# Kernel tuning notes

Measured on AMD Instinct MI355X. Metric: run time of the kernel, lower is better.

Reference implementation:

```python
import jax, jax.numpy as jnp
import numpy as np

B, N = 16, 16384
K = 16        # num_keypoints
LATENT = 128
CAGE = 8
BN_EPS = 1e-5


def setup_inputs():
    key = jax.random.key(0)
    ks = jax.random.split(key, 40)
    def rn(i, shape, s=1.0):
        return jax.random.normal(ks[i], shape, dtype=jnp.float32) * s
    inp = {
        "source_points": rn(0, (B, N, 3)),
        "target_points": rn(1, (B, N, 3)),
        "enc_w1": rn(2, (64, 3), 0.3), "enc_b1": rn(3, (64,), 0.1),
        "bn1_gamma": 1.0 + rn(4, (64,), 0.1), "bn1_beta": rn(5, (64,), 0.1),
        "bn1_mean": rn(6, (64,), 0.1), "bn1_var": 0.5 + jax.random.uniform(ks[7], (64,), dtype=jnp.float32),
        "enc_w2": rn(8, (128, 64), 0.1), "enc_b2": rn(9, (128,), 0.1),
        "bn2_gamma": 1.0 + rn(10, (128,), 0.1), "bn2_beta": rn(11, (128,), 0.1),
        "bn2_mean": rn(12, (128,), 0.1), "bn2_var": 0.5 + jax.random.uniform(ks[13], (128,), dtype=jnp.float32),
        "enc_w3": rn(14, (LATENT, 128), 0.1), "enc_b3": rn(15, (LATENT,), 0.1),
        "bn3_gamma": 1.0 + rn(16, (LATENT,), 0.1), "bn3_beta": rn(17, (LATENT,), 0.1),
        "bn3_mean": rn(18, (LATENT,), 0.1), "bn3_var": 0.5 + jax.random.uniform(ks[19], (LATENT,), dtype=jnp.float32),
        "kp_w1": rn(20, (128, LATENT), 0.1), "kp_b1": rn(21, (128,), 0.1),
        "kp_w2": rn(22, (K * 3, 128), 0.1), "kp_b2": rn(23, (K * 3,), 0.1),
        "cg_w1": rn(24, (128, K * 3), 0.1), "cg_b1": rn(25, (128,), 0.1),
        "cg_w2": rn(26, (CAGE ** 3 * 3, 128), 0.05), "cg_b2": rn(27, (CAGE ** 3 * 3,), 0.01),
    }
    return inp


def _bn(x, g, b, m, v):
    # inference-mode BatchNorm1d over channel (last) dim
    return (x - m) * jax.lax.rsqrt(v + BN_EPS) * g + b


def _encode(pts, w1, b1, g1, be1, m1, v1, w2, b2, g2, be2, m2, v2, w3, b3, g3, be3, m3, v3):
    # pointwise 1x1 convs == per-point linear layers; pts: (B, N, 3)
    h = jax.nn.relu(_bn(jnp.einsum('bnc,oc->bno', pts, w1) + b1, g1, be1, m1, v1))
    h = jax.nn.relu(_bn(jnp.einsum('bnc,oc->bno', h, w2) + b2, g2, be2, m2, v2))
    h = jax.nn.relu(_bn(jnp.einsum('bnc,oc->bno', h, w3) + b3, g3, be3, m3, v3))
    return h.max(axis=1)  # global max-pool -> (B, LATENT)


def _fps_one(pts, kps):
    # pts: (N,3), kps: (K,3). Same math as the torch loop: iterative farthest-point
    # selection; recomputing cdist to selected[:i] each step == incremental min-dist.
    # squared distances preserve argmax/min of euclidean distances.
    d0 = jnp.sum((pts[:, None, :] - kps[None, :, :]) ** 2, -1).min(axis=1)
    sel0 = pts[jnp.argmax(d0)]
    mind = jnp.sum((pts - sel0) ** 2, -1)
    def step(mind, _):
        sel = pts[jnp.argmax(mind)]
        return jnp.minimum(mind, jnp.sum((pts - sel) ** 2, -1)), sel
    _, sels = jax.lax.scan(step, mind, None, length=K - 1)
    return jnp.concatenate([sel0[None], sels], axis=0)  # (K, 3)


def _fps(points, keypoints):
    return jax.vmap(_fps_one)(points, keypoints)


def _cage_deform(pts, disp):
    # pts: (B,N,3), disp: (B,C,C,C,3). Batched trilinear interpolation on the cage.
    C = CAGE
    lin = jnp.linspace(0.0, 1.0, C)
    grid = jnp.stack(jnp.meshgrid(lin, lin, lin, indexing='ij'), axis=-1)
    cage = grid[None] + disp
    cf = cage.reshape(cage.shape[0], C * C * C, 3)
    pmin = pts.min(axis=1, keepdims=True)
    pmax = pts.max(axis=1, keepdims=True)
    t = (pts - pmin) / (pmax - pmin + 1e-6) * (C - 1)
    idx = jnp.clip(t.astype(jnp.int32), 0, C - 2)   # trunc == floor (t >= 0)
    w = t - idx.astype(t.dtype)
    u, v, z = idx[..., 0], idx[..., 1], idx[..., 2]
    wx, wy, wz = w[..., 0:1], w[..., 1:2], w[..., 2:3]
    def corner(du, dv, dz):
        flat = (u + du) * C * C + (v + dv) * C + (z + dz)      # (B,N)
        flat = jnp.broadcast_to(flat[..., None], flat.shape + (3,))
        return jnp.take_along_axis(cf, flat, axis=1)            # (B,N,3)
    d = ((1 - wx) * (1 - wy) * (1 - wz) * corner(0, 0, 0)
         + wx * (1 - wy) * (1 - wz) * corner(1, 0, 0)
         + (1 - wx) * wy * (1 - wz) * corner(0, 1, 0)
         + wx * wy * (1 - wz) * corner(1, 1, 0)
         + (1 - wx) * (1 - wy) * wz * corner(0, 0, 1)
         + wx * (1 - wy) * wz * corner(1, 0, 1)
         + (1 - wx) * wy * wz * corner(0, 1, 1)
         + wx * wy * wz * corner(1, 1, 1))
    return pts + d


def reference(source_points, target_points, enc_w1, enc_b1, bn1_gamma, bn1_beta, bn1_mean, bn1_var, enc_w2, enc_b2, bn2_gamma, bn2_beta, bn2_mean, bn2_var, enc_w3, enc_b3, bn3_gamma, bn3_beta, bn3_mean, bn3_var, kp_w1, kp_b1, kp_w2, kp_b2, cg_w1, cg_b1, cg_w2, cg_b2):
    enc = lambda p: _encode(p, enc_w1, enc_b1, bn1_gamma, bn1_beta, bn1_mean, bn1_var,
                            enc_w2, enc_b2, bn2_gamma, bn2_beta, bn2_mean, bn2_var,
                            enc_w3, enc_b3, bn3_gamma, bn3_beta, bn3_mean, bn3_var)
    src_lat = enc(source_points)
    tgt_lat = enc(target_points)
    kp = lambda lat: (jax.nn.relu(lat @ kp_w1.T + kp_b1) @ kp_w2.T + kp_b2).reshape(-1, K, 3)
    src_kp = _fps(source_points, kp(src_lat))
    tgt_kp = _fps(target_points, kp(tgt_lat))
    diff = (tgt_kp - src_kp).reshape(-1, K * 3)
    disp = (jax.nn.relu(diff @ cg_w1.T + cg_b1) @ cg_w2.T + cg_b2).reshape(-1, CAGE, CAGE, CAGE, 3)
    deformed = _cage_deform(source_points, disp)
    return (deformed, src_kp, tgt_kp)
```

## Files before the change

### kernel.cpp

```cpp
#include <hip/hip_runtime.h>

#define B_ 16
#define N_ 16384
#define K_ 16

enum : int {
  WS_LAT  = 0,
  WS_SEL  = 5632,
  WS_PMIN = 7168,
  WS_PMAX = 7216,
  WS_CF   = 7264,
  WS_W1F  = 31840,
  WS_B1F  = 32032,
  WS_WB2H = 32096,
  WS_WB2L = 36192,
  WS_B2F  = 40288,
  WS_WB3H = 40416,
  WS_B3F  = 56800,
  WS_WB3L = 56928,
  WS_END  = 73312
};

enum : int { OUT_DEF=0, OUT_SRCKP=786432, OUT_TGTKP=787200 };

typedef _Float16 f16x8 __attribute__((ext_vector_type(8)));
typedef _Float16 f16x2 __attribute__((ext_vector_type(2)));
typedef float    f32x4 __attribute__((ext_vector_type(4)));

__device__ __forceinline__ float dist2rn(float px,float py,float pz,float sx,float sy,float sz){
  float dx=__fsub_rn(px,sx), dy=__fsub_rn(py,sy), dz=__fsub_rn(pz,sz);
  return __fadd_rn(__fadd_rn(__fmul_rn(dx,dx),__fmul_rn(dy,dy)),__fmul_rn(dz,dz));
}

struct EncW {
  const float *w1,*b1,*g1,*be1,*m1,*v1;
  const float *w2,*b2,*g2,*be2,*m2,*v2;
  const float *w3,*b3,*g3,*be3,*m3,*v3;
};

__device__ __forceinline__ float bn_scale(const float* g, const float* v, int ch){
  return g[ch] * (1.0f / sqrtf(v[ch] + 1e-5f));
}

__global__ void prep_kernel(EncW a, float* ws){
  const int stride = gridDim.x*blockDim.x;
  const int tid = blockIdx.x*blockDim.x + threadIdx.x;
  for (int i=tid;i<4096;i+=stride)
    ws[WS_LAT+i] = 0.0f;
  for (int i=tid;i<192;i+=stride){
    int o=i/3;
    ws[WS_W1F+i] = a.w1[i] * bn_scale(a.g1,a.v1,o);
  }
  for (int i=tid;i<64;i+=stride){
    float s = bn_scale(a.g1,a.v1,i);
    ws[WS_B1F+i] = (a.b1[i] - a.m1[i])*s + a.be1[i];
  }
  for (int i=tid;i<8192;i+=stride){
    int j = i & 7, frag = i >> 3;
    int l = frag & 63, nk = frag >> 6;
    int kt = nk & 1, nt = nk >> 1;
    int c = kt*32 + ((l>>4)<<3) + j;
    int o = nt*16 + (l&15);
    float v = a.w2[o*64+c] * bn_scale(a.g2,a.v2,o);
    _Float16 h = (_Float16)v;
    ((_Float16*)(ws+WS_WB2H))[i] = h;
    ((_Float16*)(ws+WS_WB2L))[i] = (_Float16)(v - (float)h);
  }
  for (int i=tid;i<128;i+=stride){
    float s = bn_scale(a.g2,a.v2,i);
    ws[WS_B2F+i] = (a.b2[i] - a.m2[i])*s + a.be2[i];
  }
  for (int i=tid;i<32768;i+=stride){
    int j = i & 7, frag = i >> 3;
    int l = frag & 63, nk = frag >> 6;
    int kt = nk & 3, nt = nk >> 2;
    int c = kt*32 + ((l>>4)<<3) + j;
    int o = nt*16 + (l&15);
    float v = a.w3[o*128+c] * bn_scale(a.g3,a.v3,o);
    _Float16 h = (_Float16)v;
    ((_Float16*)(ws+WS_WB3H))[i] = h;
    ((_Float16*)(ws+WS_WB3L))[i] = (_Float16)(v - (float)h);
  }
  for (int i=tid;i<128;i+=stride){
    float s = bn_scale(a.g3,a.v3,i);
    ws[WS_B3F+i] = (a.b3[i] - a.m3[i])*s + a.be3[i];
  }
}

__global__ __launch_bounds__(256, 5) void encode_kernel(const float* __restrict__ src,
                                                        const float* __restrict__ tgt,
                                                        const float* __restrict__ ws,
                                                        float* __restrict__ lat){
  const int cloud = blockIdx.y;
  const int tile  = blockIdx.x;
  const int t = threadIdx.x;
  const int lane = t & 63;
  const int wn = __builtin_amdgcn_readfirstlane(t >> 6);
  const int lr = lane & 15;
  const int lg = lane >> 4;

  __shared__ alignas(16) _Float16 A[16384];

  const float* base = ((cloud < B_) ? (src + (size_t)cloud*N_*3)
                                    : (tgt + (size_t)(cloud-B_)*N_*3))
                      + (size_t)tile*64*3;

  f16x8 b2h[2][2], b2l[2][2];
  {
    const _Float16* wb2h = (const _Float16*)(ws + WS_WB2H);
    const _Float16* wb2l = (const _Float16*)(ws + WS_WB2L);
    #pragma unroll
    for (int kt=0; kt<2; kt++){
      #pragma unroll
      for (int n=0; n<2; n++){
        const int fi = (((wn*2+n)*2 + kt)*64 + lane)*8;
        b2h[kt][n] = *(const f16x8*)(wb2h + fi);
        b2l[kt][n] = *(const f16x8*)(wb2l + fi);
      }
    }
  }

  {
    const int pt = t >> 2, q = t & 3;
    const float x = base[pt*3+0], y = base[pt*3+1], z = base[pt*3+2];
    const float* w1 = ws + WS_W1F;
    const float* b1 = ws + WS_B1F;
    const int swz1 = (pt & 7) << 3;
    _Float16* AH1 = A;
    _Float16* AL1 = A + 4096;
    #pragma unroll
    for (int cc = 0; cc < 16; cc += 2){
      const int o = q*16 + cc;
      float v0 = fmaf(w1[o*3+2], z, fmaf(w1[o*3+1], y, w1[o*3+0]*x)) + b1[o];
      float v1 = fmaf(w1[o*3+5], z, fmaf(w1[o*3+4], y, w1[o*3+3]*x)) + b1[o+1];
      v0 = fmaxf(v0, 0.0f); v1 = fmaxf(v1, 0.0f);
      f16x2 h, l;
      h[0] = (_Float16)v0;              h[1] = (_Float16)v1;
      l[0] = (_Float16)(v0 - (float)h[0]); l[1] = (_Float16)(v1 - (float)h[1]);
      const int idx = (pt*64 + o) ^ swz1;
      *(f16x2*)&AH1[idx] = h;
      *(f16x2*)&AL1[idx] = l;
    }
  }
  __syncthreads();

  const int swz = (lr & 7) << 3;

  f32x4 acc2[4][2];
  #pragma unroll
  for (int m=0;m<4;m++){
    #pragma unroll
    for (int n=0;n<2;n++) acc2[m][n] = (f32x4){0.f,0.f,0.f,0.f};
  }
  {
    const char* pA0 = (const char*)A + lr*128 + ((( 0 + lg*8) ^ swz) << 1);
    const char* pA1 = (const char*)A + lr*128 + (((32 + lg*8) ^ swz) << 1);
    #pragma unroll
    for (int kt=0; kt<2; kt++){
      const char* pA = kt ? pA1 : pA0;
      #pragma unroll
      for (int m=0;m<4;m++){
        const f16x8 ah = *(const f16x8*)(pA + m*2048);
        const f16x8 al = *(const f16x8*)(pA + m*2048 + 8192);
        #pragma unroll
        for (int n=0;n<2;n++){
          acc2[m][n] = __builtin_amdgcn_mfma_f32_16x16x32_f16(ah, b2h[kt][n], acc2[m][n], 0,0,0);
          acc2[m][n] = __builtin_amdgcn_mfma_f32_16x16x32_f16(ah, b2l[kt][n], acc2[m][n], 0,0,0);
          acc2[m][n] = __builtin_amdgcn_mfma_f32_16x16x32_f16(al, b2h[kt][n], acc2[m][n], 0,0,0);
        }
      }
    }
  }
  __syncthreads();

  {
    #pragma unroll
    for (int n=0;n<2;n++){
      const int ch = wn*32 + n*16 + lr;
      const float b = ws[WS_B2F + ch];
      #pragma unroll
      for (int r=0;r<4;r++){
        const int mask = ((lg*4 + r) & 7) << 3;
        char* pW = (char*)A + ((ch ^ mask) << 1) + lg*1024 + r*256;
        #pragma unroll
        for (int m=0;m<4;m++){
          const float v = fmaxf(acc2[m][n][r] + b, 0.0f);
          const _Float16 hi = (_Float16)v;
          const _Float16 lo = (_Float16)(v - (float)hi);
          *(_Float16*)(pW + m*4096) = hi;
          *(_Float16*)(pW + m*4096 + 16384) = lo;
        }
      }
    }
  }
  __syncthreads();

  f32x4 acc3[4][2];
  #pragma unroll
  for (int m=0;m<4;m++){
    #pragma unroll
    for (int n=0;n<2;n++) acc3[m][n] = (f32x4){0.f,0.f,0.f,0.f};
  }
  {
    const _Float16* wb3h = (const _Float16*)(ws + WS_WB3H);
    const _Float16* wb3l = (const _Float16*)(ws + WS_WB3L);
    const char* pR = (const char*)A + lr*256;
    #pragma unroll
    for (int kt=0; kt<4; kt++){
      f16x8 bh[2], bl[2];
      #pragma unroll
      for (int n=0;n<2;n++){
        const int fi = (((wn*2+n)*4 + kt)*64 + lane)*8;
        bh[n] = *(const f16x8*)(wb3h + fi);
        bl[n] = *(const f16x8*)(wb3l + fi);
      }
      const int c3 = ((kt*32 + lg*8) ^ swz) << 1;
      #pragma unroll
      for (int m=0;m<4;m++){
        const f16x8 ah = *(const f16x8*)(pR + c3 + m*4096);
        const f16x8 al = *(const f16x8*)(pR + c3 + m*4096 + 16384);
        #pragma unroll
        for (int n=0;n<2;n++){
          acc3[m][n] = __builtin_amdgcn_mfma_f32_16x16x32_f16(ah, bh[n], acc3[m][n], 0,0,0);
          acc3[m][n] = __builtin_amdgcn_mfma_f32_16x16x32_f16(ah, bl[n], acc3[m][n], 0,0,0);
          acc3[m][n] = __builtin_amdgcn_mfma_f32_16x16x32_f16(al, bh[n], acc3[m][n], 0,0,0);
        }
      }
    }
  }

  {
    const float* b3 = ws + WS_B3F;
    #pragma unroll
    for (int n=0;n<2;n++){
      const int ch = wn*32 + n*16 + lr;
      const float b = b3[ch];
      float x = 0.0f;
      #pragma unroll
      for (int m=0;m<4;m++){
        #pragma unroll
        for (int r=0;r<4;r++)
          x = fmaxf(x, acc3[m][n][r] + b);
      }
      x = fmaxf(x, __shfl_xor(x, 16, 64));
      x = fmaxf(x, __shfl_xor(x, 32, 64));
      if (lane < 16)
        atomicMax((unsigned*)(lat + cloud*128 + ch), __float_as_uint(x));
    }
  }
}

__device__ __forceinline__ void fps_round(int r, int t, int wv,
                                          float bv, int bi, float bx, float by, float bz,
                                          float (*cv)[16], int (*ci)[16],
                                          float (*cx)[16], float (*cy)[16], float (*cz)[16],
                                          float* ws, float* out, int cloud,
                                          float& s0, float& s1, float& s2){
  float v = bv; int i = bi;
  #pragma unroll
  for (int m=1;m<64;m<<=1){
    float v2=__shfl_xor(v,m,64); int i2=__shfl_xor(i,m,64);
    if (v2 > v || (v2 == v && i2 < i)){ v=v2; i=i2; }
  }
  const int p = r & 1;
  if ((i >> 4) == t){ cv[p][wv]=v; ci[p][wv]=i; cx[p][wv]=bx; cy[p][wv]=by; cz[p][wv]=bz; }
  __syncthreads();
  float wvv = cv[p][0]; int wi = ci[p][0]; int slot = 0;
  #pragma unroll
  for (int e=1;e<16;e++){
    float v2=cv[p][e]; int i2=ci[p][e];
    if (v2 > wvv || (v2 == wvv && i2 < wi)){ wvv=v2; wi=i2; slot=e; }
  }
  s0 = cx[p][slot]; s1 = cy[p][slot]; s2 = cz[p][slot];
  if (t == 0){
    float* sw = ws + WS_SEL + cloud*48 + r*3;
    sw[0]=s0; sw[1]=s1; sw[2]=s2;
    size_t o = (cloud<B_) ? (size_t)(OUT_SRCKP + cloud*48 + r*3)
                          : (size_t)(OUT_TGTKP + (cloud-B_)*48 + r*3);
    out[o]=s0; out[o+1]=s1; out[o+2]=s2;
  }
}

__global__ __launch_bounds__(1024, 4) void fps_kernel(const float* __restrict__ src,
                                                      const float* __restrict__ tgt,
                                                      const float* __restrict__ kw1,
                                                      const float* __restrict__ kb1,
                                                      const float* __restrict__ kw2,
                                                      const float* __restrict__ kb2,
                                                      float* ws, float* out){
  const int cloud = blockIdx.x; const int t = threadIdx.x;
  const int wv = t >> 6;
  const int lane = t & 63;
  const float* base = (cloud < B_) ? (src + (size_t)cloud*N_*3)
                                   : (tgt + (size_t)cloud*N_*3 - (size_t)B_*N_*3);
  __shared__ float kpl[48];
  __shared__ float h[128];
  __shared__ float cv[2][16]; __shared__ int ci[2][16];
  __shared__ float cx[2][16]; __shared__ float cy[2][16]; __shared__ float cz[2][16];
  __shared__ float red[96];

  float px[16], py[16], pz[16];
  {
    const float4* b4 = (const float4*)(base + (size_t)t*48);
    #pragma unroll
    for (int q=0;q<4;q++){
      float4 va=b4[q*3], vb=b4[q*3+1], vc=b4[q*3+2];
      px[q*4  ]=va.x; py[q*4  ]=va.y; pz[q*4  ]=va.z;
      px[q*4+1]=va.w; py[q*4+1]=vb.x; pz[q*4+1]=vb.y;
      px[q*4+2]=vb.z; py[q*4+2]=vb.w; pz[q*4+2]=vc.x;
      px[q*4+3]=vc.y; py[q*4+3]=vc.z; pz[q*4+3]=vc.w;
    }
  }

  if (cloud < B_){
    float mn0=3.4e38f,mn1=3.4e38f,mn2=3.4e38f, mx0=-3.4e38f,mx1=-3.4e38f,mx2=-3.4e38f;
    #pragma unroll
    for (int k=0;k<16;k++){
      mn0=fminf(mn0,px[k]); mn1=fminf(mn1,py[k]); mn2=fminf(mn2,pz[k]);
      mx0=fmaxf(mx0,px[k]); mx1=fmaxf(mx1,py[k]); mx2=fmaxf(mx2,pz[k]);
    }
    #pragma unroll
    for (int m=1;m<64;m<<=1){
      mn0=fminf(mn0,__shfl_xor(mn0,m,64)); mx0=fmaxf(mx0,__shfl_xor(mx0,m,64));
      mn1=fminf(mn1,__shfl_xor(mn1,m,64)); mx1=fmaxf(mx1,__shfl_xor(mx1,m,64));
      mn2=fminf(mn2,__shfl_xor(mn2,m,64)); mx2=fmaxf(mx2,__shfl_xor(mx2,m,64));
    }
    if (lane==0){
      red[wv*6+0]=mn0; red[wv*6+1]=mn1; red[wv*6+2]=mn2;
      red[wv*6+3]=mx0; red[wv*6+4]=mx1; red[wv*6+5]=mx2;
    }
    __syncthreads();
    if (t < 6){
      float v = red[t];
      for (int e=1;e<16;e++){
        float v2 = red[e*6+t];
        v = (t<3) ? fminf(v,v2) : fmaxf(v,v2);
      }
      if (t<3) ws[WS_PMIN + cloud*3 + t] = v;
      else     ws[WS_PMAX + cloud*3 + (t-3)] = v;
    }
  }
  __syncthreads();

  const float* lat = ws + WS_LAT + cloud*128;
  if (t < 128){
    float acc = kb1[t];
    const float* w = kw1 + t*128;
    for (int c=0;c<128;c++) acc = fmaf(lat[c], w[c], acc);
    h[t] = fmaxf(acc, 0.0f);
  }
  __syncthreads();
  if (t < 48){
    float acc = kb2[t];
    const float* w = kw2 + t*128;
    for (int c=0;c<128;c++) acc = fmaf(h[c], w[c], acc);
    kpl[t] = acc;
  }
  __syncthreads();

  float mind[16];
  #pragma unroll
  for (int k=0;k<16;k++) mind[k] = 3.4028235e38f;
  for (int j=0;j<K_;j++){
    const float sx=kpl[j*3], sy=kpl[j*3+1], sz=kpl[j*3+2];
    #pragma unroll
    for (int k=0;k<16;k++)
      mind[k] = fminf(mind[k], dist2rn(px[k],py[k],pz[k], sx,sy,sz));
  }

  float bv = -1.0f; int bi = 0; float bx=0.f, by=0.f, bz=0.f;
  #pragma unroll
  for (int k=0;k<16;k++){
    if (mind[k] > bv){ bv=mind[k]; bi=t*16+k; bx=px[k]; by=py[k]; bz=pz[k]; }
  }
  float s0, s1, s2;
  fps_round(0, t, wv, bv, bi, bx, by, bz, cv, ci, cx, cy, cz, ws, out, cloud, s0, s1, s2);

  bv = -1.0f; bi = 0;
  #pragma unroll
  for (int k=0;k<16;k++){
    float d = dist2rn(px[k],py[k],pz[k], s0,s1,s2);
    mind[k] = d;
    if (d > bv){ bv=d; bi=t*16+k; bx=px[k]; by=py[k]; bz=pz[k]; }
  }
  fps_round(1, t, wv, bv, bi, bx, by, bz, cv, ci, cx, cy, cz, ws, out, cloud, s0, s1, s2);

  for (int r=2; r<K_; ++r){
    bv = -1.0f; bi = 0;
    #pragma unroll
    for (int k=0;k<16;k++){
      float d = dist2rn(px[k],py[k],pz[k], s0,s1,s2);
      float m = fminf(mind[k], d);
      mind[k] = m;
      if (m > bv){ bv=m; bi=t*16+k; bx=px[k]; by=py[k]; bz=pz[k]; }
    }
    fps_round(r, t, wv, bv, bi, bx, by, bz, cv, ci, cx, cy, cz, ws, out, cloud, s0, s1, s2);
  }
}

__global__ __launch_bounds__(256) void deform_kernel(const float* __restrict__ src,
                                                     const float* __restrict__ cw1,
                                                     const float* __restrict__ cb1,
                                                     const float* __restrict__ cw2,
                                                     const float* __restrict__ cb2,
                                                     const float* __restrict__ ws,
                                                     float* __restrict__ out){
  const int b = blockIdx.y;
  const int t = threadIdx.x;
  __shared__ float cf[1536];
  __shared__ float diff[48];
  __shared__ float hh[128];

  if (t<48) diff[t] = __fsub_rn(ws[WS_SEL + (B_+b)*48 + t], ws[WS_SEL + b*48 + t]);
  __syncthreads();
  if (t<128){
    const float* w = cw1 + t*48;
    float acc = cb1[t];
    for (int j=0;j<48;j++) acc = fmaf(diff[j], w[j], acc);
    hh[t] = fmaxf(acc, 0.0f);
  }
  __syncthreads();
  for (int o = t; o < 1536; o += 256){
    const float* w = cw2 + o*128;
    float acc = cb2[o];
    for (int c=0;c<128;c++) acc = fmaf(hh[c], w[c], acc);
    int flat = o/3, coord = o - flat*3;
    int u = flat>>6, v=(flat>>3)&7, z=flat&7;
    int g = (coord==0)?u:((coord==1)?v:z);
    float gv = (g==7)?1.0f:(float)g*(1.0f/7.0f);
    cf[o] = gv + acc;
  }
  __syncthreads();

  const float mn0 = ws[WS_PMIN+b*3+0], mn1 = ws[WS_PMIN+b*3+1], mn2 = ws[WS_PMIN+b*3+2];
  const float mx0 = ws[WS_PMAX+b*3+0], mx1 = ws[WS_PMAX+b*3+1], mx2 = ws[WS_PMAX+b*3+2];

  #pragma unroll
  for (int k=0;k<4;k++){
    const int n = blockIdx.x*1024 + k*256 + t;
    const float* p = src + ((size_t)b*N_ + n)*3;
    float pt[3]; int id[3]; float w[3];
    #pragma unroll
    for (int c=0;c<3;c++){
      float pv = p[c];
      float mnv = (c==0)?mn0:((c==1)?mn1:mn2);
      float mxv = (c==0)?mx0:((c==1)?mx1:mx2);
      float denom = __fadd_rn(__fsub_rn(mxv, mnv), 1e-6f);
      float tc = __fmul_rn(__fdiv_rn(__fsub_rn(pv, mnv), denom), 7.0f);
      int ic = (int)tc; ic = min(max(ic,0),6);
      pt[c]=pv; id[c]=ic; w[c]=__fsub_rn(tc, (float)ic);
    }
    const int flat = (id[0]<<6) + (id[1]<<3) + id[2];
    const float* c000 = cf + flat*3;
    const float wx=w[0], wy=w[1], wz=w[2];
    const float ux=__fsub_rn(1.0f,wx), uy=__fsub_rn(1.0f,wy), uz=__fsub_rn(1.0f,wz);
    const float w000=__fmul_rn(__fmul_rn(ux,uy),uz);
    const float w100=__fmul_rn(__fmul_rn(wx,uy),uz);
    const float w010=__fmul_rn(__fmul_rn(ux,wy),uz);
    const float w110=__fmul_rn(__fmul_rn(wx,wy),uz);
    const float w001=__fmul_rn(__fmul_rn(ux,uy),wz);
    const float w101=__fmul_rn(__fmul_rn(wx,uy),wz);
    const float w011=__fmul_rn(__fmul_rn(ux,wy),wz);
    const float w111=__fmul_rn(__fmul_rn(wx,wy),wz);
    #pragma unroll
    for (int c=0;c<3;c++){
      float d = __fmul_rn(w000, c000[c]);
      d = __fadd_rn(d, __fmul_rn(w100, c000[192+c]));
      d = __fadd_rn(d, __fmul_rn(w010, c000[24+c]));
      d = __fadd_rn(d, __fmul_rn(w110, c000[216+c]));
      d = __fadd_rn(d, __fmul_rn(w001, c000[3+c]));
      d = __fadd_rn(d, __fmul_rn(w101, c000[195+c]));
      d = __fadd_rn(d, __fmul_rn(w011, c000[27+c]));
      d = __fadd_rn(d, __fmul_rn(w111, c000[219+c]));
      out[((size_t)b*N_+n)*3 + c] = __fadd_rn(pt[c], d);
    }
  }
}

extern "C" void kernel_launch(void* const* d_in, const int* in_sizes, int n_in,
                              void* d_out, int out_size, void* d_ws, size_t ws_size,
                              hipStream_t stream){
  const float* src = (const float*)d_in[0];
  const float* tgt = (const float*)d_in[1];
  float* ws = (float*)d_ws;
  float* out = (float*)d_out;

  EncW ew;
  ew.w1 =(const float*)d_in[2];  ew.b1 =(const float*)d_in[3];
  ew.g1 =(const float*)d_in[4];  ew.be1=(const float*)d_in[5];
  ew.m1 =(const float*)d_in[6];  ew.v1 =(const float*)d_in[7];
  ew.w2 =(const float*)d_in[8];  ew.b2 =(const float*)d_in[9];
  ew.m2 =(const float*)d_in[12]; ew.v2 =(const float*)d_in[13];
  ew.g2 =(const float*)d_in[10]; ew.be2=(const float*)d_in[11];
  ew.w3 =(const float*)d_in[14]; ew.b3 =(const float*)d_in[15];
  ew.g3 =(const float*)d_in[16]; ew.be3=(const float*)d_in[17];
  ew.m3 =(const float*)d_in[18]; ew.v3 =(const float*)d_in[19];

  prep_kernel<<<128, 256, 0, stream>>>(ew, ws);
  encode_kernel<<<dim3(256,32), 256, 0, stream>>>(src, tgt, ws, ws + WS_LAT);
  fps_kernel<<<32, 1024, 0, stream>>>(src, tgt,
      (const float*)d_in[20], (const float*)d_in[21],
      (const float*)d_in[22], (const float*)d_in[23], ws, out);
  deform_kernel<<<dim3(16,16), 256, 0, stream>>>(src,
      (const float*)d_in[24], (const float*)d_in[25],
      (const float*)d_in[26], (const float*)d_in[27], ws, out);
}
```

Baseline: 298.4 us.

## Switch encoder GEMMs from 16x16x32 to 32x32x16 MFMA tiles

```diff
diff --git a/kernel.cpp b/kernel.cpp
--- a/kernel.cpp
+++ b/kernel.cpp
@@ -25,7 +25,7 @@
 
 typedef _Float16 f16x8 __attribute__((ext_vector_type(8)));
 typedef _Float16 f16x2 __attribute__((ext_vector_type(2)));
-typedef float    f32x4 __attribute__((ext_vector_type(4)));
+typedef float    f32x16 __attribute__((ext_vector_type(16)));
 
 __device__ __forceinline__ float dist2rn(float px,float py,float pz,float sx,float sy,float sz){
   float dx=__fsub_rn(px,sx), dy=__fsub_rn(py,sy), dz=__fsub_rn(pz,sz);
@@ -57,10 +57,10 @@
   }
   for (int i=tid;i<8192;i+=stride){
     int j = i & 7, frag = i >> 3;
-    int l = frag & 63, nk = frag >> 6;
-    int kt = nk & 1, nt = nk >> 1;
-    int c = kt*32 + ((l>>4)<<3) + j;
-    int o = nt*16 + (l&15);
+    int l = frag & 63, wk = frag >> 6;
+    int kt = wk & 3, wn = wk >> 2;
+    int c = kt*16 + ((l>>5)<<3) + j;
+    int o = wn*32 + (l&31);
     float v = a.w2[o*64+c] * bn_scale(a.g2,a.v2,o);
     _Float16 h = (_Float16)v;
     ((_Float16*)(ws+WS_WB2H))[i] = h;
@@ -70,12 +70,12 @@
     float s = bn_scale(a.g2,a.v2,i);
     ws[WS_B2F+i] = (a.b2[i] - a.m2[i])*s + a.be2[i];
   }
-  for (int i=tid;i<32768;i+=stride){
+  for (int i=tid;i<16384;i+=stride){
     int j = i & 7, frag = i >> 3;
-    int l = frag & 63, nk = frag >> 6;
-    int kt = nk & 3, nt = nk >> 2;
-    int c = kt*32 + ((l>>4)<<3) + j;
-    int o = nt*16 + (l&15);
+    int l = frag & 63, wk = frag >> 6;
+    int kt = wk & 7, wn = wk >> 3;
+    int c = kt*16 + ((l>>5)<<3) + j;
+    int o = wn*32 + (l&31);
     float v = a.w3[o*128+c] * bn_scale(a.g3,a.v3,o);
     _Float16 h = (_Float16)v;
     ((_Float16*)(ws+WS_WB3H))[i] = h;
@@ -96,8 +96,9 @@
   const int t = threadIdx.x;
   const int lane = t & 63;
   const int wn = __builtin_amdgcn_readfirstlane(t >> 6);
-  const int lr = lane & 15;
-  const int lg = lane >> 4;
+  const int l31 = lane & 31;
+  const int hb  = lane >> 5;
+  const int swz = (l31 & 7) << 3;
 
   __shared__ alignas(16) _Float16 A[16384];
 
@@ -105,18 +106,15 @@
                                     : (tgt + (size_t)(cloud-B_)*N_*3))
                       + (size_t)tile*64*3;
 
-  f16x8 b2h[2][2], b2l[2][2];
+  f16x8 b2h[4], b2l[4];
   {
     const _Float16* wb2h = (const _Float16*)(ws + WS_WB2H);
     const _Float16* wb2l = (const _Float16*)(ws + WS_WB2L);
     #pragma unroll
-    for (int kt=0; kt<2; kt++){
-      #pragma unroll
-      for (int n=0; n<2; n++){
-        const int fi = (((wn*2+n)*2 + kt)*64 + lane)*8;
-        b2h[kt][n] = *(const f16x8*)(wb2h + fi);
-        b2l[kt][n] = *(const f16x8*)(wb2l + fi);
-      }
+    for (int kt=0; kt<4; kt++){
+      const int fi = ((wn*4 + kt)*64 + lane)*8;
+      b2h[kt] = *(const f16x8*)(wb2h + fi);
+      b2l[kt] = *(const f16x8*)(wb2l + fi);
     }
   }
 
@@ -142,111 +140,93 @@
       *(f16x2*)&AL1[idx] = l;
     }
   }
-  __syncthreads();
-
-  const int swz = (lr & 7) << 3;
-
-  f32x4 acc2[4][2];
-  #pragma unroll
-  for (int m=0;m<4;m++){
-    #pragma unroll
-    for (int n=0;n<2;n++) acc2[m][n] = (f32x4){0.f,0.f,0.f,0.f};
-  }
-  {
-    const char* pA0 = (const char*)A + lr*128 + ((( 0 + lg*8) ^ swz) << 1);
-    const char* pA1 = (const char*)A + lr*128 + (((32 + lg*8) ^ swz) << 1);
-    #pragma unroll
-    for (int kt=0; kt<2; kt++){
-      const char* pA = kt ? pA1 : pA0;
+
+  int koff[8];
+  #pragma unroll
+  for (int kt=0; kt<8; kt++) koff[kt] = (((kt*16) | (hb*8)) ^ swz) << 1;
+
+  __syncthreads();
+
+  f32x16 acc2[2];
+  #pragma unroll
+  for (int e=0;e<16;e++){ acc2[0][e]=0.0f; acc2[1][e]=0.0f; }
+  {
+    const char* pA2 = (const char*)A + l31*128;
+    #pragma unroll
+    for (int kt=0; kt<4; kt++){
       #pragma unroll
-      for (int m=0;m<4;m++){
-        const f16x8 ah = *(const f16x8*)(pA + m*2048);
-        const f16x8 al = *(const f16x8*)(pA + m*2048 + 8192);
+      for (int m=0;m<2;m++){
+        const f16x8 ah = *(const f16x8*)(pA2 + m*4096 + koff[kt]);
+        const f16x8 al = *(const f16x8*)(pA2 + m*4096 + koff[kt] + 8192);
+        acc2[m] = __builtin_amdgcn_mfma_f32_32x32x16_f16(ah, b2h[kt], acc2[m], 0,0,0);
+        acc2[m] = __builtin_amdgcn_mfma_f32_32x32x16_f16(ah, b2l[kt], acc2[m], 0,0,0);
+        acc2[m] = __builtin_amdgcn_mfma_f32_32x32x16_f16(al, b2h[kt], acc2[m], 0,0,0);
+      }
+    }
+  }
+  __syncthreads();
+
+  const int ch = wn*32 + l31;
+  {
+    const float b = ws[WS_B2F + ch];
+    char* pWr[4];
+    #pragma unroll
+    for (int r4=0;r4<4;r4++)
+      pWr[r4] = (char*)A + (r4 + 4*hb)*256 + ((ch ^ ((r4 + 4*hb) << 3)) << 1);
+    #pragma unroll
+    for (int r4=0;r4<4;r4++){
+      #pragma unroll
+      for (int rq=0;rq<4;rq++){
+        const int reg = rq*4 + r4;
         #pragma unroll
-        for (int n=0;n<2;n++){
-          acc2[m][n] = __builtin_amdgcn_mfma_f32_16x16x32_f16(ah, b2h[kt][n], acc2[m][n], 0,0,0);
-          acc2[m][n] = __builtin_amdgcn_mfma_f32_16x16x32_f16(ah, b2l[kt][n], acc2[m][n], 0,0,0);
-          acc2[m][n] = __builtin_amdgcn_mfma_f32_16x16x32_f16(al, b2h[kt][n], acc2[m][n], 0,0,0);
+        for (int m=0;m<2;m++){
+          const float v = fmaxf(acc2[m][reg] + b, 0.0f);
+          const _Float16 hi = (_Float16)v;
+          const _Float16 lo = (_Float16)(v - (float)hi);
+          char* pw = pWr[r4] + rq*2048 + m*8192;
+          *(_Float16*)(pw) = hi;
+          *(_Float16*)(pw + 16384) = lo;
         }
       }
     }
   }
   __syncthreads();
 
-  {
-    #pragma unroll
-    for (int n=0;n<2;n++){
-      const int ch = wn*32 + n*16 + lr;
-      const float b = ws[WS_B2F + ch];
-      #pragma unroll
-      for (int r=0;r<4;r++){
-        const int mask = ((lg*4 + r) & 7) << 3;
-        char* pW = (char*)A + ((ch ^ mask) << 1) + lg*1024 + r*256;
-        #pragma unroll
-        for (int m=0;m<4;m++){
-          const float v = fmaxf(acc2[m][n][r] + b, 0.0f);
-          const _Float16 hi = (_Float16)v;
-          const _Float16 lo = (_Float16)(v - (float)hi);
-          *(_Float16*)(pW + m*4096) = hi;
-          *(_Float16*)(pW + m*4096 + 16384) = lo;
-        }
-      }
-    }
-  }
-  __syncthreads();
-
-  f32x4 acc3[4][2];
-  #pragma unroll
-  for (int m=0;m<4;m++){
-    #pragma unroll
-    for (int n=0;n<2;n++) acc3[m][n] = (f32x4){0.f,0.f,0.f,0.f};
-  }
+  f32x16 acc3[2];
+  #pragma unroll
+  for (int e=0;e<16;e++){ acc3[0][e]=0.0f; acc3[1][e]=0.0f; }
   {
     const _Float16* wb3h = (const _Float16*)(ws + WS_WB3H);
     const _Float16* wb3l = (const _Float16*)(ws + WS_WB3L);
-    const char* pR = (const char*)A + lr*256;
-    #pragma unroll
-    for (int kt=0; kt<4; kt++){
-      f16x8 bh[2], bl[2];
+    const char* pA3 = (const char*)A + l31*256;
+    #pragma unroll
+    for (int kt=0; kt<8; kt++){
+      const int fi = ((wn*8 + kt)*64 + lane)*8;
+      const f16x8 bh = *(const f16x8*)(wb3h + fi);
+      const f16x8 bl = *(const f16x8*)(wb3l + fi);
       #pragma unroll
-      for (int n=0;n<2;n++){
-        const int fi = (((wn*2+n)*4 + kt)*64 + lane)*8;
-        bh[n] = *(const f16x8*)(wb3h + fi);
-        bl[n] = *(const f16x8*)(wb3l + fi);
+      for (int m=0;m<2;m++){
+        const f16x8 ah = *(const f16x8*)(pA3 + m*8192 + koff[kt]);
+        const f16x8 al = *(const f16x8*)(pA3 + m*8192 + koff[kt] + 16384);
+        acc3[m] = __builtin_amdgcn_mfma_f32_32x32x16_f16(ah, bh, acc3[m], 0,0,0);
+        acc3[m] = __builtin_amdgcn_mfma_f32_32x32x16_f16(ah, bl, acc3[m], 0,0,0);
+        acc3[m] = __builtin_amdgcn_mfma_f32_32x32x16_f16(al, bh, acc3[m], 0,0,0);
       }
-      const int c3 = ((kt*32 + lg*8) ^ swz) << 1;
+    }
+  }
+
+  {
+    const float b = ws[WS_B3F + ch];
+    float x = 0.0f;
+    #pragma unroll
+    for (int m=0;m<2;m++){
       #pragma unroll
-      for (int m=0;m<4;m++){
-        const f16x8 ah = *(const f16x8*)(pR + c3 + m*4096);
-        const f16x8 al = *(const f16x8*)(pR + c3 + m*4096 + 16384);
-        #pragma unroll
-        for (int n=0;n<2;n++){
-          acc3[m][n] = __builtin_amdgcn_mfma_f32_16x16x32_f16(ah, bh[n], acc3[m][n], 0,0,0);
-          acc3[m][n] = __builtin_amdgcn_mfma_f32_16x16x32_f16(ah, bl[n], acc3[m][n], 0,0,0);
-          acc3[m][n] = __builtin_amdgcn_mfma_f32_16x16x32_f16(al, bh[n], acc3[m][n], 0,0,0);
-        }
-      }
-    }
-  }
-
-  {
-    const float* b3 = ws + WS_B3F;
-    #pragma unroll
-    for (int n=0;n<2;n++){
-      const int ch = wn*32 + n*16 + lr;
-      const float b = b3[ch];
-      float x = 0.0f;
-      #pragma unroll
-      for (int m=0;m<4;m++){
-        #pragma unroll
-        for (int r=0;r<4;r++)
-          x = fmaxf(x, acc3[m][n][r] + b);
-      }
-      x = fmaxf(x, __shfl_xor(x, 16, 64));
-      x = fmaxf(x, __shfl_xor(x, 32, 64));
-      if (lane < 16)
-        atomicMax((unsigned*)(lat + cloud*128 + ch), __float_as_uint(x));
-    }
+      for (int r=0;r<16;r++)
+        x = fmaxf(x, acc3[m][r] + b);
+    }
+    x = fmaxf(x, __shfl_xor(x, 32, 64));
+    if (lane < 32)
+      atomicMax((unsigned*)(lat + cloud*128 + ch), __float_as_uint(x));
   }
 }
 
@@ -490,8 +470,8 @@
   ew.g1 =(const float*)d_in[4];  ew.be1=(const float*)d_in[5];
   ew.m1 =(const float*)d_in[6];  ew.v1 =(const float*)d_in[7];
   ew.w2 =(const float*)d_in[8];  ew.b2 =(const float*)d_in[9];
+  ew.g2 =(const float*)d_in[10]; ew.be2=(const float*)d_in[11];
   ew.m2 =(const float*)d_in[12]; ew.v2 =(const float*)d_in[13];
-  ew.g2 =(const float*)d_in[10]; ew.be2=(const float*)d_in[11];
   ew.w3 =(const float*)d_in[14]; ew.b3 =(const float*)d_in[15];
   ew.g3 =(const float*)d_in[16]; ew.be3=(const float*)d_in[17];
   ew.m3 =(const float*)d_in[18]; ew.v3 =(const float*)d_in[19];
```

Result: no change. 297.9 us (-0.2%).
